# Performance work log

Hardware: AMD Instinct MI355X
Metric: run time of the kernel (lower is better)

## Reference

```python
import jax, jax.numpy as jnp
import numpy as np

B, W, S, D, H = 16, 128, 16, 768, 12
HD = D // H

def _ln(x, g, b):
    m = x.mean(-1, keepdims=True)
    v = ((x - m) ** 2).mean(-1, keepdims=True)
    return (x - m) / jnp.sqrt(v + 1e-5) * g + b

def _lin(x, w, b):
    return x @ w.T + b

def _rope(t):
    # t: (N, H, L, HD); interleaved even/odd rotation, base 10000
    inv = 1.0 / (10000.0 ** (jnp.arange(0, HD, 2, dtype=jnp.float32) / HD))
    fr = jnp.arange(t.shape[2], dtype=jnp.float32)[:, None] * inv[None, :]  # (L, HD//2)
    cos, sin = jnp.cos(fr), jnp.sin(fr)
    te, to = t[..., ::2], t[..., 1::2]
    return jnp.stack([te * cos - to * sin, te * sin + to * cos], -1).reshape(t.shape)

def _mha(q, k, v, mask=None):
    # q,k,v: (N, H, L, HD)
    s = jnp.einsum('nhqd,nhkd->nhqk', q, k) / jnp.sqrt(jnp.float32(HD))
    if mask is not None:
        s = jnp.where(mask[None, None], -jnp.inf, s)
    a = jax.nn.softmax(s, axis=-1)
    return jnp.einsum('nhqk,nhkd->nhqd', a, v)

def _heads(t, L):
    return t.reshape(-1, L, H, HD).transpose(0, 2, 1, 3)

def setup_inputs() -> dict:
    key = jax.random.key(0)
    ks = jax.random.split(key, 16)
    def w(i, shape):
        return jax.random.normal(ks[i], shape, jnp.float32) * 0.02
    return {
        'x': jax.random.normal(ks[0], (B, W, S, D), jnp.float32),
        'causal_mask': jnp.triu(jnp.ones((W, W), dtype=bool), k=1),
        'sn_g': jnp.ones((D,), jnp.float32), 'sn_b': jnp.zeros((D,), jnp.float32),
        'sa_in_w': w(1, (3 * D, D)), 'sa_in_b': jnp.zeros((3 * D,), jnp.float32),
        'sa_out_w': w(2, (D, D)), 'sa_out_b': jnp.zeros((D,), jnp.float32),
        'tn_g': jnp.ones((D,), jnp.float32), 'tn_b': jnp.zeros((D,), jnp.float32),
        'tq_w': w(3, (D, D)), 'tq_b': jnp.zeros((D,), jnp.float32),
        'tk_w': w(4, (D, D)), 'tk_b': jnp.zeros((D,), jnp.float32),
        'tv_w': w(5, (D, D)), 'tv_b': jnp.zeros((D,), jnp.float32),
        'to_w': w(6, (D, D)), 'to_b': jnp.zeros((D,), jnp.float32),
        'fn_g': jnp.ones((D,), jnp.float32), 'fn_b': jnp.zeros((D,), jnp.float32),
        'f1_w': w(7, (4 * D, D)), 'f1_b': jnp.zeros((4 * D,), jnp.float32),
        'f2_w': w(8, (D, 4 * D)), 'f2_b': jnp.zeros((D,), jnp.float32),
    }

def reference(x, causal_mask, sn_g, sn_b, sa_in_w, sa_in_b, sa_out_w, sa_out_b,
              tn_g, tn_b, tq_w, tq_b, tk_w, tk_b, tv_w, tv_b, to_w, to_b,
              fn_g, fn_b, f1_w, f1_b, f2_w, f2_b):
    # ---- spatial attention within each timestep: (B*W, S, D) ----
    xs = x.reshape(B * W, S, D)
    xn = _ln(xs, sn_g, sn_b)
    q, k, v = jnp.split(_lin(xn, sa_in_w, sa_in_b), 3, axis=-1)
    o = _mha(_heads(q, S), _heads(k, S), _heads(v, S))
    o = o.transpose(0, 2, 1, 3).reshape(B * W, S, D)
    xs = xs + _lin(o, sa_out_w, sa_out_b)
    x = xs.reshape(B, W, S, D)
    # ---- causal temporal attention with RoPE: (B*S, W, D) ----
    xt = x.transpose(0, 2, 1, 3).reshape(B * S, W, D)
    xn = _ln(xt, tn_g, tn_b)
    q = _rope(_heads(_lin(xn, tq_w, tq_b), W))
    k = _rope(_heads(_lin(xn, tk_w, tk_b), W))
    v = _heads(_lin(xn, tv_w, tv_b), W)
    o = _mha(q, k, v, causal_mask)
    o = o.transpose(0, 2, 1, 3).reshape(B * S, W, D)
    xt = xt + _lin(o, to_w, to_b)
    x = xt.reshape(B, S, W, D).transpose(0, 2, 1, 3)
    # ---- feed-forward (exact GELU, as torch default) ----
    h = jax.nn.gelu(_lin(_ln(x, fn_g, fn_b), f1_w, f1_b), approximate=False)
    return x + _lin(h, f2_w, f2_b)
```

## Files before the change

### kernel.cpp

```cpp
#include <hip/hip_runtime.h>
#include <stdint.h>


#define NB 16
#define NW 128
#define NS 16
#define ND 768
#define NH 12
#define NTOK 32768

typedef __attribute__((ext_vector_type(8))) short short8;
typedef __attribute__((ext_vector_type(4))) float f32x4;

__device__ __forceinline__ float blo(unsigned v){ return __builtin_bit_cast(float, v << 16); }
__device__ __forceinline__ float bhi(unsigned v){ return __builtin_bit_cast(float, v & 0xffff0000u); }
__device__ __forceinline__ float bus(unsigned short u){ return __builtin_bit_cast(float, ((unsigned)u) << 16); }
__device__ __forceinline__ unsigned short f2b(float f){
  unsigned u = __builtin_bit_cast(unsigned, f);
  u += 0x7fffu + ((u >> 16) & 1u);
  return (unsigned short)(u >> 16);
}
__device__ __forceinline__ void gld_lds16(const void* g, void* l){
  __builtin_amdgcn_global_load_lds((const __attribute__((address_space(1))) void*)g,
                                   (__attribute__((address_space(3))) void*)l, 16, 0, 0);
}

__global__ __launch_bounds__(256) void convert_k(const float* __restrict__ in,
                                                 unsigned short* __restrict__ out, int n4){
  int i = blockIdx.x * 256 + threadIdx.x;
  int stride = gridDim.x * 256;
  for (; i < n4; i += stride){
    float4 v = ((const float4*)in)[i];
    unsigned lo = (unsigned)f2b(v.x) | ((unsigned)f2b(v.y) << 16);
    unsigned hi = (unsigned)f2b(v.z) | ((unsigned)f2b(v.w) << 16);
    ((uint2*)out)[i] = make_uint2(lo, hi);
  }
}

__global__ __launch_bounds__(256) void concat3_k(const float* __restrict__ a, const float* __restrict__ b,
                                                 const float* __restrict__ c, float* __restrict__ o){
  int i = blockIdx.x * 256 + threadIdx.x;
  if (i < 768){ o[i] = a[i]; o[768 + i] = b[i]; o[1536 + i] = c[i]; }
}

__global__ __launch_bounds__(256) void rope_k(float* __restrict__ tab){
  int i = blockIdx.x * 256 + threadIdx.x;
  if (i < 128 * 32){
    int w = i >> 5, p = i & 31;
    float inv = powf(10000.0f, -((float)(2 * p)) / 64.0f);
    float ang = (float)w * inv;
    tab[i * 2] = cosf(ang);
    tab[i * 2 + 1] = sinf(ang);
  }
}

template<int INF32>
__global__ __launch_bounds__(256) void ln_k(const void* __restrict__ xin, const float* __restrict__ g,
                                            const float* __restrict__ bt, unsigned short* __restrict__ out){
  const int row = blockIdx.x;
  const int t = threadIdx.x;
  const float* xf = (const float*)xin;
  const unsigned short* xb = (const unsigned short*)xin;
  float v[3];
#pragma unroll
  for (int i = 0; i < 3; ++i){
    int j = t + i * 256;
    v[i] = INF32 ? xf[(size_t)row * 768 + j] : bus(xb[(size_t)row * 768 + j]);
  }
  float s = v[0] + v[1] + v[2];
  float ss = v[0]*v[0] + v[1]*v[1] + v[2]*v[2];
#pragma unroll
  for (int o = 1; o < 64; o <<= 1){ s += __shfl_xor(s, o, 64); ss += __shfl_xor(ss, o, 64); }
  __shared__ float red[8];
  int w = t >> 6;
  if ((t & 63) == 0){ red[w*2] = s; red[w*2+1] = ss; }
  __syncthreads();
  s = red[0] + red[2] + red[4] + red[6];
  ss = red[1] + red[3] + red[5] + red[7];
  float mean = s * (1.0f / 768.0f);
  float var = ss * (1.0f / 768.0f) - mean * mean;
  float rstd = rsqrtf(var + 1e-5f);
#pragma unroll
  for (int i = 0; i < 3; ++i){
    int j = t + i * 256;
    out[(size_t)row * 768 + j] = f2b((v[i] - mean) * rstd * g[j] + bt[j]);
  }
}

template<int MODE>
__global__ __launch_bounds__(512) void gemm256_k(const unsigned short* __restrict__ A,
                                                 const unsigned short* __restrict__ Bw,
                                                 const float* __restrict__ bias,
                                                 const void* __restrict__ resid,
                                                 void* __restrict__ outp, int K, int M){
  __shared__ char LB[131072];
  char* const Asl = LB;
  char* const Bsl = LB + 65536;
  const int tid = threadIdx.x;
  const int lane = tid & 63, w = tid >> 6;
  const int llo = lane & 15, lhi = lane >> 4;
  const int wm = w >> 2, wn = w & 3;
  const int brow = blockIdx.y << 8, bcol = blockIdx.x << 8;
  const int NT = K >> 6;

  auto stage = [&](const unsigned short* __restrict__ g, int row0, int t, int half, char* slotbase){
    const int r0 = tid >> 3, cp = tid & 7;
#pragma unroll
    for (int j = 0; j < 2; ++j){
      const int r = r0 + (j << 6);
      const unsigned short* src = g + (size_t)(row0 + half * 128 + r) * K + t * 64;
      gld_lds16((const char*)src + ((cp << 4) ^ ((r & 7) << 4)),
                slotbase + (w << 10) + (j << 13));
    }
  };

  stage(A,  brow, 0, 0, Asl);
  stage(A,  brow, 0, 1, Asl + (1 << 14));
  stage(Bw, bcol, 0, 0, Bsl);
  stage(Bw, bcol, 0, 1, Bsl + (1 << 14));
  stage(A,  brow, 1, 0, Asl + (2 << 14));
  stage(A,  brow, 1, 1, Asl + (3 << 14));
  asm volatile("s_waitcnt vmcnt(4)" ::: "memory");
  __builtin_amdgcn_s_barrier();

  f32x4 acc[8][4];
#pragma unroll
  for (int m = 0; m < 8; ++m)
#pragma unroll
    for (int n = 0; n < 4; ++n) acc[m][n] = f32x4{0.f, 0.f, 0.f, 0.f};

  for (int t = 0; t < NT; ++t){
    const char* Ab = Asl + (((2 * t + wm) & 3) << 14);
    const char* Bb = Bsl + (((2 * t + (wn >> 1)) & 3) << 14);

    short8 a[8][2];
#pragma unroll
    for (int m = 0; m < 8; ++m){
      const int rr = (m << 4) + llo;
#pragma unroll
      for (int ks = 0; ks < 2; ++ks)
        a[m][ks] = *(const short8*)(Ab + rr * 128 + (((ks << 6) + (lhi << 4)) ^ ((rr & 7) << 4)));
    }

#pragma unroll
    for (int n = 0; n < 4; ++n){
      const int cc = ((wn & 1) << 6) + (n << 4) + llo;
      short8 b0 = *(const short8*)(Bb + cc * 128 + ((lhi << 4) ^ ((cc & 7) << 4)));
      short8 b1 = *(const short8*)(Bb + cc * 128 + ((64 + (lhi << 4)) ^ ((cc & 7) << 4)));
      if (n == 1 && t + 1 < NT){
        stage(Bw, bcol, t + 1, 0, Bsl + (((2 * t + 2) & 3) << 14));
        stage(Bw, bcol, t + 1, 1, Bsl + (((2 * t + 3) & 3) << 14));
      }
      if (n == 2 && t + 2 < NT)
        stage(A, brow, t + 2, 0, Asl + (((2 * t + 4) & 3) << 14));
      if (n == 3 && t + 2 < NT)
        stage(A, brow, t + 2, 1, Asl + (((2 * t + 5) & 3) << 14));
      __builtin_amdgcn_s_barrier();
      asm volatile("s_waitcnt lgkmcnt(0)" ::: "memory");
      __builtin_amdgcn_s_setprio(1);
#pragma unroll
      for (int m = 0; m < 8; ++m){
        acc[m][n] = __builtin_amdgcn_mfma_f32_16x16x32_bf16(b0, a[m][0], acc[m][n], 0, 0, 0);
        acc[m][n] = __builtin_amdgcn_mfma_f32_16x16x32_bf16(b1, a[m][1], acc[m][n], 0, 0, 0);
      }
      __builtin_amdgcn_s_setprio(0);
      if (n == 3){
        if (t + 2 < NT) asm volatile("s_waitcnt vmcnt(4)" ::: "memory");
        else            asm volatile("s_waitcnt vmcnt(0)" ::: "memory");
      }
      __builtin_amdgcn_s_barrier();
    }
  }

  const int orow = brow + (wm << 7);
  const int ocol = bcol + (wn << 6);
  const unsigned short* resb = (const unsigned short*)resid;
  const float* resf = (const float*)resid;
#pragma unroll
  for (int m = 0; m < 8; ++m){
    const int row = orow + (m << 4) + llo;
    const size_t rb = (size_t)row * M;
#pragma unroll
    for (int n = 0; n < 4; ++n){
      const int col = ocol + (n << 4) + (lhi << 2);
      const float4 bv = *(const float4*)&bias[col];
      float v0 = acc[m][n][0] + bv.x;
      float v1 = acc[m][n][1] + bv.y;
      float v2 = acc[m][n][2] + bv.z;
      float v3 = acc[m][n][3] + bv.w;
      const size_t off = rb + col;
      if (MODE == 1){
        v0 = 0.5f * v0 * (1.0f + erff(v0 * 0.70710678118654752f));
        v1 = 0.5f * v1 * (1.0f + erff(v1 * 0.70710678118654752f));
        v2 = 0.5f * v2 * (1.0f + erff(v2 * 0.70710678118654752f));
        v3 = 0.5f * v3 * (1.0f + erff(v3 * 0.70710678118654752f));
      } else if (MODE == 2){
        const float4 rv = *(const float4*)&resf[off];
        v0 += rv.x; v1 += rv.y; v2 += rv.z; v3 += rv.w;
      } else if (MODE == 3 || MODE == 4){
        const uint2 rv = *(const uint2*)&resb[off];
        v0 += blo(rv.x); v1 += bhi(rv.x); v2 += blo(rv.y); v3 += bhi(rv.y);
      }
      if (MODE == 4){
        float4 ov; ov.x = v0; ov.y = v1; ov.z = v2; ov.w = v3;
        *(float4*)&((float*)outp)[off] = ov;
      } else {
        unsigned lo = (unsigned)f2b(v0) | ((unsigned)f2b(v1) << 16);
        unsigned hi = (unsigned)f2b(v2) | ((unsigned)f2b(v3) << 16);
        *(uint2*)&((unsigned short*)outp)[off] = make_uint2(lo, hi);
      }
    }
  }
}

__global__ __launch_bounds__(256) void sattn_k(const unsigned short* __restrict__ qkv,
                                               unsigned short* __restrict__ o){
  const int bw = blockIdx.x, h = blockIdx.y;
  const int t = threadIdx.x;
  __shared__ unsigned short qh[16 * 68], kh[16 * 68], vh[16 * 68];
  __shared__ float pl[16 * 17];
  const int row = t >> 4, c4 = t & 15;
  const size_t base = ((size_t)(bw * 16 + row)) * 2304 + h * 64 + c4 * 4;
  *(uint2*)&qh[row * 68 + c4 * 4] = *(const uint2*)&qkv[base];
  *(uint2*)&kh[row * 68 + c4 * 4] = *(const uint2*)&qkv[base + 768];
  *(uint2*)&vh[row * 68 + c4 * 4] = *(const uint2*)&qkv[base + 1536];
  __syncthreads();

  const int q = row, k = c4;
  float s = 0.f;
#pragma unroll
  for (int c = 0; c < 16; ++c){
    uint2 qv = *(const uint2*)&qh[q * 68 + c * 4];
    uint2 kv = *(const uint2*)&kh[k * 68 + c * 4];
    s += blo(qv.x) * blo(kv.x) + bhi(qv.x) * bhi(kv.x);
    s += blo(qv.y) * blo(kv.y) + bhi(qv.y) * bhi(kv.y);
  }
  s *= 0.125f;
  float m = s;
#pragma unroll
  for (int off = 1; off < 16; off <<= 1) m = fmaxf(m, __shfl_xor(m, off, 64));
  float p = __expf(s - m);
  float su = p;
#pragma unroll
  for (int off = 1; off < 16; off <<= 1) su += __shfl_xor(su, off, 64);
  pl[q * 17 + k] = p / su;
  __syncthreads();

  float o0 = 0.f, o1 = 0.f, o2 = 0.f, o3 = 0.f;
#pragma unroll
  for (int kk = 0; kk < 16; ++kk){
    float pw = pl[q * 17 + kk];
    uint2 vv = *(const uint2*)&vh[kk * 68 + c4 * 4];
    o0 += pw * blo(vv.x); o1 += pw * bhi(vv.x);
    o2 += pw * blo(vv.y); o3 += pw * bhi(vv.y);
  }
  const size_t ob = ((size_t)(bw * 16 + q)) * 768 + h * 64 + c4 * 4;
  unsigned r0 = (unsigned)f2b(o0) | ((unsigned)f2b(o1) << 16);
  unsigned r1 = (unsigned)f2b(o2) | ((unsigned)f2b(o3) << 16);
  *(uint2*)&o[ob] = make_uint2(r0, r1);
}

__global__ __launch_bounds__(256) void tattn_k(const unsigned short* __restrict__ qkv,
                                               const float* __restrict__ rope,
                                               unsigned short* __restrict__ o){
  const int bs = blockIdx.x, h = blockIdx.y;
  const int b = bs >> 4, s = bs & 15;
  const int t = threadIdx.x, lane = t & 63, w = t >> 6;
  const int lhi = lane >> 4, llo = lane & 15;
  __shared__ unsigned short Qs[128 * 64];
  __shared__ unsigned short Ks[128 * 64];
  __shared__ unsigned short Vt[64 * 128];
  __shared__ unsigned short P[128 * 128];

  {
    const int r = t >> 1;
    const int dbase = (t & 1) * 32;
    const size_t tokb = ((size_t)((b * 128 + r) * 16 + s)) * 2304 + h * 64;
    const float2* rp = (const float2*)rope;
#pragma unroll
    for (int mch = 0; mch < 4; ++mch){
      const int d0 = dbase + mch * 8;
      uint4 qv = *(const uint4*)&qkv[tokb + d0];
      uint4 kv = *(const uint4*)&qkv[tokb + 768 + d0];
      uint4 vv = *(const uint4*)&qkv[tokb + 1536 + d0];
      unsigned qin[4] = {qv.x, qv.y, qv.z, qv.w};
      unsigned kin[4] = {kv.x, kv.y, kv.z, kv.w};
      unsigned qo[4], ko[4];
#pragma unroll
      for (int j = 0; j < 4; ++j){
        float2 cssn = rp[r * 32 + (d0 >> 1) + j];
        float cs = cssn.x, sn = cssn.y;
        float qe = blo(qin[j]), qd = bhi(qin[j]);
        float ke = blo(kin[j]), kd = bhi(kin[j]);
        qo[j] = (unsigned)f2b(qe * cs - qd * sn) | ((unsigned)f2b(qe * sn + qd * cs) << 16);
        ko[j] = (unsigned)f2b(ke * cs - kd * sn) | ((unsigned)f2b(ke * sn + kd * cs) << 16);
      }
      const int byq = r * 128 + ((d0 * 2) ^ ((r & 7) << 4));
      *(uint4*)((char*)Qs + byq) = make_uint4(qo[0], qo[1], qo[2], qo[3]);
      *(uint4*)((char*)Ks + byq) = make_uint4(ko[0], ko[1], ko[2], ko[3]);
      unsigned vin[4] = {vv.x, vv.y, vv.z, vv.w};
#pragma unroll
      for (int j = 0; j < 8; ++j){
        const int d = d0 + j;
        unsigned short val = (j & 1) ? (unsigned short)(vin[j >> 1] >> 16)
                                     : (unsigned short)(vin[j >> 1] & 0xffffu);
        *(unsigned short*)((char*)Vt + d * 256 + ((r * 2) ^ ((d & 7) << 4))) = val;
      }
    }
  }
  __syncthreads();

  const int qbase = w * 32;
  f32x4 st[8][2];
#pragma unroll
  for (int i = 0; i < 8; ++i){ st[i][0] = f32x4{0.f,0.f,0.f,0.f}; st[i][1] = f32x4{0.f,0.f,0.f,0.f}; }
#pragma unroll
  for (int kd = 0; kd < 2; ++kd){
    short8 bq[2];
#pragma unroll
    for (int fq = 0; fq < 2; ++fq){
      const int qr = qbase + fq * 16 + llo;
      bq[fq] = *(const short8*)((const char*)Qs + qr * 128 + ((kd * 64 + lhi * 16) ^ ((qr & 7) << 4)));
    }
#pragma unroll
    for (int fk = 0; fk < 8; ++fk){
      const int kr = fk * 16 + llo;
      short8 ak = *(const short8*)((const char*)Ks + kr * 128 + ((kd * 64 + lhi * 16) ^ ((kr & 7) << 4)));
      st[fk][0] = __builtin_amdgcn_mfma_f32_16x16x32_bf16(ak, bq[0], st[fk][0], 0, 0, 0);
      st[fk][1] = __builtin_amdgcn_mfma_f32_16x16x32_bf16(ak, bq[1], st[fk][1], 0, 0, 0);
    }
  }

#pragma unroll
  for (int fq = 0; fq < 2; ++fq){
    const int qg = qbase + fq * 16 + llo;
    float m = -1e30f;
#pragma unroll
    for (int fk = 0; fk < 8; ++fk)
#pragma unroll
      for (int rr = 0; rr < 4; ++rr){
        const int kg = fk * 16 + lhi * 4 + rr;
        float sv = (kg <= qg) ? st[fk][fq][rr] : -1e30f;
        st[fk][fq][rr] = sv;
        m = fmaxf(m, sv);
      }
    m = fmaxf(m, __shfl_xor(m, 16, 64));
    m = fmaxf(m, __shfl_xor(m, 32, 64));
    float su = 0.f;
#pragma unroll
    for (int fk = 0; fk < 8; ++fk)
#pragma unroll
      for (int rr = 0; rr < 4; ++rr){
        float p = __expf((st[fk][fq][rr] - m) * 0.125f);
        st[fk][fq][rr] = p;
        su += p;
      }
    su += __shfl_xor(su, 16, 64);
    su += __shfl_xor(su, 32, 64);
    const float rs = 1.0f / su;
#pragma unroll
    for (int fk = 0; fk < 8; ++fk){
      const int kk = fk * 16 + lhi * 4;
      unsigned lo = (unsigned)f2b(st[fk][fq][0] * rs) | ((unsigned)f2b(st[fk][fq][1] * rs) << 16);
      unsigned hi = (unsigned)f2b(st[fk][fq][2] * rs) | ((unsigned)f2b(st[fk][fq][3] * rs) << 16);
      *(uint2*)((char*)P + qg * 256 + ((kk * 2) ^ ((qg & 7) << 4))) = make_uint2(lo, hi);
    }
  }
  __syncthreads();

  f32x4 oacc[2][4];
#pragma unroll
  for (int i = 0; i < 2; ++i)
#pragma unroll
    for (int j = 0; j < 4; ++j) oacc[i][j] = f32x4{0.f,0.f,0.f,0.f};
#pragma unroll
  for (int ks = 0; ks < 4; ++ks){
    short8 pa[2];
#pragma unroll
    for (int fq = 0; fq < 2; ++fq){
      const int qr = qbase + fq * 16 + llo;
      pa[fq] = *(const short8*)((const char*)P + qr * 256 + ((ks * 64 + lhi * 16) ^ ((qr & 7) << 4)));
    }
#pragma unroll
    for (int fd = 0; fd < 4; ++fd){
      const int dr = fd * 16 + llo;
      short8 vb = *(const short8*)((const char*)Vt + dr * 256 + ((ks * 64 + lhi * 16) ^ ((dr & 7) << 4)));
      oacc[0][fd] = __builtin_amdgcn_mfma_f32_16x16x32_bf16(pa[0], vb, oacc[0][fd], 0, 0, 0);
      oacc[1][fd] = __builtin_amdgcn_mfma_f32_16x16x32_bf16(pa[1], vb, oacc[1][fd], 0, 0, 0);
    }
  }

#pragma unroll
  for (int fq = 0; fq < 2; ++fq)
#pragma unroll
    for (int fd = 0; fd < 4; ++fd)
#pragma unroll
      for (int rr = 0; rr < 4; ++rr){
        const int qg = qbase + fq * 16 + lhi * 4 + rr;
        const int d = fd * 16 + llo;
        const size_t ob = ((size_t)((b * 128 + qg) * 16 + s)) * 768 + h * 64 + d;
        o[ob] = f2b(oacc[fq][fd][rr]);
      }
}

__global__ __launch_bounds__(256) void sentinel_k(float* out){
  if (blockIdx.x == 0 && threadIdx.x == 0) out[0] = 12345.0f;
}

extern "C" void kernel_launch(void* const* d_in, const int* in_sizes, int n_in,
                              void* d_out, int out_size, void* d_ws, size_t ws_size,
                              hipStream_t stream){
  const float* x       = (const float*)d_in[0];
  const float* sn_g    = (const float*)d_in[2];
  const float* sn_b    = (const float*)d_in[3];
  const float* sa_in_w = (const float*)d_in[4];
  const float* sa_in_b = (const float*)d_in[5];
  const float* sa_out_w= (const float*)d_in[6];
  const float* sa_out_b= (const float*)d_in[7];
  const float* tn_g    = (const float*)d_in[8];
  const float* tn_b    = (const float*)d_in[9];
  const float* tq_w    = (const float*)d_in[10];
  const float* tq_b    = (const float*)d_in[11];
  const float* tk_w    = (const float*)d_in[12];
  const float* tk_b    = (const float*)d_in[13];
  const float* tv_w    = (const float*)d_in[14];
  const float* tv_b    = (const float*)d_in[15];
  const float* to_w    = (const float*)d_in[16];
  const float* to_b    = (const float*)d_in[17];
  const float* fn_g    = (const float*)d_in[18];
  const float* fn_b    = (const float*)d_in[19];
  const float* f1_w    = (const float*)d_in[20];
  const float* f1_b    = (const float*)d_in[21];
  const float* f2_w    = (const float*)d_in[22];
  const float* f2_b    = (const float*)d_in[23];

  char* ws = (char*)d_ws;
  size_t off = 0;
  auto alloc = [&](size_t bytes) -> void* {
    void* p = ws + off;
    off += (bytes + 255) & ~(size_t)255;
    return p;
  };
  unsigned short* Wqkv = (unsigned short*)alloc((size_t)2304*768*2);
  unsigned short* Wo1  = (unsigned short*)alloc((size_t)768*768*2);
  unsigned short* W3   = (unsigned short*)alloc((size_t)2304*768*2);
  float*          b3   = (float*)alloc(2304*4);
  unsigned short* Wto  = (unsigned short*)alloc((size_t)768*768*2);
  unsigned short* Wf1  = (unsigned short*)alloc((size_t)3072*768*2);
  unsigned short* Wf2  = (unsigned short*)alloc((size_t)768*3072*2);
  float*          rope = (float*)alloc(128*32*2*4);
  unsigned short* xn   = (unsigned short*)alloc((size_t)NTOK*768*2);
  unsigned short* qkv  = (unsigned short*)alloc((size_t)NTOK*3072*2);
  unsigned short* xs2  = (unsigned short*)alloc((size_t)NTOK*768*2);
  unsigned short* xt2  = (unsigned short*)alloc((size_t)NTOK*768*2);
  unsigned short* ob   = xn;

  if (ws_size < off){ sentinel_k<<<1, 64, 0, stream>>>((float*)d_out); return; }

  convert_k<<<1024, 256, 0, stream>>>(sa_in_w, Wqkv, 2304*768/4);
  convert_k<<<512, 256, 0, stream>>>(sa_out_w, Wo1, 768*768/4);
  convert_k<<<512, 256, 0, stream>>>(tq_w, W3, 768*768/4);
  convert_k<<<512, 256, 0, stream>>>(tk_w, W3 + 768*768, 768*768/4);
  convert_k<<<512, 256, 0, stream>>>(tv_w, W3 + 2*768*768, 768*768/4);
  concat3_k<<<3, 256, 0, stream>>>(tq_b, tk_b, tv_b, b3);
  convert_k<<<512, 256, 0, stream>>>(to_w, Wto, 768*768/4);
  convert_k<<<1024, 256, 0, stream>>>(f1_w, Wf1, 3072*768/4);
  convert_k<<<1024, 256, 0, stream>>>(f2_w, Wf2, 768*3072/4);
  rope_k<<<16, 256, 0, stream>>>(rope);

  ln_k<1><<<NTOK, 256, 0, stream>>>(x, sn_g, sn_b, xn);
  gemm256_k<0><<<dim3(9, 128), 512, 0, stream>>>(xn, Wqkv, sa_in_b, nullptr, qkv, 768, 2304);
  sattn_k<<<dim3(2048, 12), 256, 0, stream>>>(qkv, ob);
  gemm256_k<2><<<dim3(3, 128), 512, 0, stream>>>(ob, Wo1, sa_out_b, x, xs2, 768, 768);

  ln_k<0><<<NTOK, 256, 0, stream>>>(xs2, tn_g, tn_b, xn);
  gemm256_k<0><<<dim3(9, 128), 512, 0, stream>>>(xn, W3, b3, nullptr, qkv, 768, 2304);
  tattn_k<<<dim3(256, 12), 256, 0, stream>>>(qkv, rope, ob);
  gemm256_k<3><<<dim3(3, 128), 512, 0, stream>>>(ob, Wto, to_b, xs2, xt2, 768, 768);

  ln_k<0><<<NTOK, 256, 0, stream>>>(xt2, fn_g, fn_b, xn);
  gemm256_k<1><<<dim3(12, 128), 512, 0, stream>>>(xn, Wf1, f1_b, nullptr, qkv, 768, 3072);
  gemm256_k<4><<<dim3(3, 128), 512, 0, stream>>>(qkv, Wf2, f2_b, xt2, d_out, 3072, 768);
}
```

Baseline: 1.196 ms.

## Split GEMM k-step into quadrant phases and use tanh-form GELU

Result: faster. 1.141 ms (-4.7%).

```diff
diff --git a/kernel.cpp b/kernel.cpp
--- a/kernel.cpp
+++ b/kernel.cpp
@@ -103,23 +103,25 @@
   const int brow = blockIdx.y << 8, bcol = blockIdx.x << 8;
   const int NT = K >> 6;
 
-  auto stage = [&](const unsigned short* __restrict__ g, int row0, int t, int half, char* slotbase){
-    const int r0 = tid >> 3, cp = tid & 7;
-#pragma unroll
-    for (int j = 0; j < 2; ++j){
-      const int r = r0 + (j << 6);
-      const unsigned short* src = g + (size_t)(row0 + half * 128 + r) * K + t * 64;
-      gld_lds16((const char*)src + ((cp << 4) ^ ((r & 7) << 4)),
-                slotbase + (w << 10) + (j << 13));
-    }
+  const int r0 = tid >> 3, cp = tid & 7;
+  const int swz = (cp << 4) ^ ((r0 & 7) << 4);
+  const char* aG = (const char*)(A + (size_t)(brow + r0) * K) + swz;
+  const char* bG = (const char*)(Bw + (size_t)(bcol + r0) * K) + swz;
+  const int J  = K * 128;
+  const int Hh = K * 256;
+  const int ldst = w << 10;
+
+  auto stage = [&](const char* g, int gb, char* slotbase){
+    gld_lds16(g + gb,     slotbase + ldst);
+    gld_lds16(g + gb + J, slotbase + ldst + (1 << 13));
   };
 
-  stage(A,  brow, 0, 0, Asl);
-  stage(A,  brow, 0, 1, Asl + (1 << 14));
-  stage(Bw, bcol, 0, 0, Bsl);
-  stage(Bw, bcol, 0, 1, Bsl + (1 << 14));
-  stage(A,  brow, 1, 0, Asl + (2 << 14));
-  stage(A,  brow, 1, 1, Asl + (3 << 14));
+  stage(aG, 0,        Asl);
+  stage(aG, Hh,       Asl + (1 << 14));
+  stage(bG, 0,        Bsl);
+  stage(bG, Hh,       Bsl + (1 << 14));
+  stage(aG, 128,      Asl + (2 << 14));
+  stage(aG, 128 + Hh, Asl + (3 << 14));
   asm volatile("s_waitcnt vmcnt(4)" ::: "memory");
   __builtin_amdgcn_s_barrier();
 
@@ -132,44 +134,94 @@
   for (int t = 0; t < NT; ++t){
     const char* Ab = Asl + (((2 * t + wm) & 3) << 14);
     const char* Bb = Bsl + (((2 * t + (wn >> 1)) & 3) << 14);
-
-    short8 a[8][2];
-#pragma unroll
-    for (int m = 0; m < 8; ++m){
-      const int rr = (m << 4) + llo;
+    const int tb = t << 7;
+    short8 a0[4][2], a1[4][2], b0[2][2], b1[2][2];
+
+#pragma unroll
+    for (int mi = 0; mi < 4; ++mi){
+      const int rr = (mi << 4) + llo;
 #pragma unroll
       for (int ks = 0; ks < 2; ++ks)
-        a[m][ks] = *(const short8*)(Ab + rr * 128 + (((ks << 6) + (lhi << 4)) ^ ((rr & 7) << 4)));
-    }
-
-#pragma unroll
-    for (int n = 0; n < 4; ++n){
-      const int cc = ((wn & 1) << 6) + (n << 4) + llo;
-      short8 b0 = *(const short8*)(Bb + cc * 128 + ((lhi << 4) ^ ((cc & 7) << 4)));
-      short8 b1 = *(const short8*)(Bb + cc * 128 + ((64 + (lhi << 4)) ^ ((cc & 7) << 4)));
-      if (n == 1 && t + 1 < NT){
-        stage(Bw, bcol, t + 1, 0, Bsl + (((2 * t + 2) & 3) << 14));
-        stage(Bw, bcol, t + 1, 1, Bsl + (((2 * t + 3) & 3) << 14));
-      }
-      if (n == 2 && t + 2 < NT)
-        stage(A, brow, t + 2, 0, Asl + (((2 * t + 4) & 3) << 14));
-      if (n == 3 && t + 2 < NT)
-        stage(A, brow, t + 2, 1, Asl + (((2 * t + 5) & 3) << 14));
-      __builtin_amdgcn_s_barrier();
-      asm volatile("s_waitcnt lgkmcnt(0)" ::: "memory");
-      __builtin_amdgcn_s_setprio(1);
-#pragma unroll
-      for (int m = 0; m < 8; ++m){
-        acc[m][n] = __builtin_amdgcn_mfma_f32_16x16x32_bf16(b0, a[m][0], acc[m][n], 0, 0, 0);
-        acc[m][n] = __builtin_amdgcn_mfma_f32_16x16x32_bf16(b1, a[m][1], acc[m][n], 0, 0, 0);
-      }
-      __builtin_amdgcn_s_setprio(0);
-      if (n == 3){
-        if (t + 2 < NT) asm volatile("s_waitcnt vmcnt(4)" ::: "memory");
-        else            asm volatile("s_waitcnt vmcnt(0)" ::: "memory");
-      }
-      __builtin_amdgcn_s_barrier();
-    }
+        a0[mi][ks] = *(const short8*)(Ab + rr * 128 + (((ks << 6) + (lhi << 4)) ^ ((rr & 7) << 4)));
+    }
+#pragma unroll
+    for (int ni = 0; ni < 2; ++ni){
+      const int cc = ((wn & 1) << 6) + (ni << 4) + llo;
+#pragma unroll
+      for (int ks = 0; ks < 2; ++ks)
+        b0[ni][ks] = *(const short8*)(Bb + cc * 128 + (((ks << 6) + (lhi << 4)) ^ ((cc & 7) << 4)));
+    }
+    if (t + 1 < NT) stage(bG, tb + 128, Bsl + (((2 * t + 2) & 3) << 14));
+    __builtin_amdgcn_s_barrier();
+    asm volatile("s_waitcnt lgkmcnt(0)" ::: "memory");
+    __builtin_amdgcn_s_setprio(1);
+#pragma unroll
+    for (int mi = 0; mi < 4; ++mi)
+#pragma unroll
+      for (int ni = 0; ni < 2; ++ni){
+        acc[mi][ni] = __builtin_amdgcn_mfma_f32_16x16x32_bf16(b0[ni][0], a0[mi][0], acc[mi][ni], 0, 0, 0);
+        acc[mi][ni] = __builtin_amdgcn_mfma_f32_16x16x32_bf16(b0[ni][1], a0[mi][1], acc[mi][ni], 0, 0, 0);
+      }
+    __builtin_amdgcn_s_setprio(0);
+    __builtin_amdgcn_s_barrier();
+
+#pragma unroll
+    for (int mi = 0; mi < 4; ++mi){
+      const int rr = 64 + (mi << 4) + llo;
+#pragma unroll
+      for (int ks = 0; ks < 2; ++ks)
+        a1[mi][ks] = *(const short8*)(Ab + rr * 128 + (((ks << 6) + (lhi << 4)) ^ ((rr & 7) << 4)));
+    }
+    if (t + 1 < NT) stage(bG, tb + 128 + Hh, Bsl + (((2 * t + 3) & 3) << 14));
+    __builtin_amdgcn_s_barrier();
+    asm volatile("s_waitcnt lgkmcnt(0)" ::: "memory");
+    __builtin_amdgcn_s_setprio(1);
+#pragma unroll
+    for (int mi = 0; mi < 4; ++mi)
+#pragma unroll
+      for (int ni = 0; ni < 2; ++ni){
+        acc[4 + mi][ni] = __builtin_amdgcn_mfma_f32_16x16x32_bf16(b0[ni][0], a1[mi][0], acc[4 + mi][ni], 0, 0, 0);
+        acc[4 + mi][ni] = __builtin_amdgcn_mfma_f32_16x16x32_bf16(b0[ni][1], a1[mi][1], acc[4 + mi][ni], 0, 0, 0);
+      }
+    __builtin_amdgcn_s_setprio(0);
+    __builtin_amdgcn_s_barrier();
+
+#pragma unroll
+    for (int ni = 0; ni < 2; ++ni){
+      const int cc = ((wn & 1) << 6) + 32 + (ni << 4) + llo;
+#pragma unroll
+      for (int ks = 0; ks < 2; ++ks)
+        b1[ni][ks] = *(const short8*)(Bb + cc * 128 + (((ks << 6) + (lhi << 4)) ^ ((cc & 7) << 4)));
+    }
+    if (t + 2 < NT) stage(aG, tb + 256, Asl + (((2 * t + 4) & 3) << 14));
+    __builtin_amdgcn_s_barrier();
+    asm volatile("s_waitcnt lgkmcnt(0)" ::: "memory");
+    __builtin_amdgcn_s_setprio(1);
+#pragma unroll
+    for (int mi = 0; mi < 4; ++mi)
+#pragma unroll
+      for (int ni = 0; ni < 2; ++ni){
+        acc[mi][2 + ni] = __builtin_amdgcn_mfma_f32_16x16x32_bf16(b1[ni][0], a0[mi][0], acc[mi][2 + ni], 0, 0, 0);
+        acc[mi][2 + ni] = __builtin_amdgcn_mfma_f32_16x16x32_bf16(b1[ni][1], a0[mi][1], acc[mi][2 + ni], 0, 0, 0);
+      }
+    __builtin_amdgcn_s_setprio(0);
+    __builtin_amdgcn_s_barrier();
+
+    if (t + 2 < NT) stage(aG, tb + 256 + Hh, Asl + (((2 * t + 5) & 3) << 14));
+    __builtin_amdgcn_s_barrier();
+    asm volatile("s_waitcnt lgkmcnt(0)" ::: "memory");
+    __builtin_amdgcn_s_setprio(1);
+#pragma unroll
+    for (int mi = 0; mi < 4; ++mi)
+#pragma unroll
+      for (int ni = 0; ni < 2; ++ni){
+        acc[4 + mi][2 + ni] = __builtin_amdgcn_mfma_f32_16x16x32_bf16(b1[ni][0], a1[mi][0], acc[4 + mi][2 + ni], 0, 0, 0);
+        acc[4 + mi][2 + ni] = __builtin_amdgcn_mfma_f32_16x16x32_bf16(b1[ni][1], a1[mi][1], acc[4 + mi][2 + ni], 0, 0, 0);
+      }
+    __builtin_amdgcn_s_setprio(0);
+    if (t + 2 < NT) asm volatile("s_waitcnt vmcnt(4)" ::: "memory");
+    else            asm volatile("s_waitcnt vmcnt(0)" ::: "memory");
+    __builtin_amdgcn_s_barrier();
   }
 
   const int orow = brow + (wm << 7);
@@ -190,10 +242,14 @@
       float v3 = acc[m][n][3] + bv.w;
       const size_t off = rb + col;
       if (MODE == 1){
-        v0 = 0.5f * v0 * (1.0f + erff(v0 * 0.70710678118654752f));
-        v1 = 0.5f * v1 * (1.0f + erff(v1 * 0.70710678118654752f));
-        v2 = 0.5f * v2 * (1.0f + erff(v2 * 0.70710678118654752f));
-        v3 = 0.5f * v3 * (1.0f + erff(v3 * 0.70710678118654752f));
+        float y0 = v0 * (1.5957691216f + 0.0713548163f * v0 * v0);
+        float y1 = v1 * (1.5957691216f + 0.0713548163f * v1 * v1);
+        float y2 = v2 * (1.5957691216f + 0.0713548163f * v2 * v2);
+        float y3 = v3 * (1.5957691216f + 0.0713548163f * v3 * v3);
+        v0 = v0 / (1.0f + __expf(-y0));
+        v1 = v1 / (1.0f + __expf(-y1));
+        v2 = v2 / (1.0f + __expf(-y2));
+        v3 = v3 / (1.0f + __expf(-y3));
       } else if (MODE == 2){
         const float4 rv = *(const float4*)&resf[off];
         v0 += rv.x; v1 += rv.y; v2 += rv.z; v3 += rv.w;
```
